# Kernel tuning notes

Measured on AMD Instinct MI355X. Metric: run time of the kernel, lower is better.

## Reference

```python
import jax, jax.numpy as jnp
import numpy as np

H, B, N, D = 8, 256, 200, 128
KD = D // H                      # key_dim = embed_dim // n_heads = 16
TRI = N * (N - 1) // 2           # strictly upper-triangular count per matrix
NORM = 1.0 / np.sqrt(KD)
NEG = -jnp.inf


def setup_inputs() -> dict:
    key = jax.random.key(0)
    k1, k2, k3, k4, k5 = jax.random.split(key, 5)
    q = jax.random.normal(k1, (B, N, D), dtype=jnp.float32)
    che_mask = jax.random.randint(k2, (H, B, TRI), 0, 2).astype(bool)
    exchange = jax.random.randint(k3, (B, 2), 0, N)
    stdv = 1.0 / np.sqrt(KD)
    Wq = jax.random.uniform(k4, (H, D, KD), jnp.float32, -stdv, stdv)
    Wk = jax.random.uniform(k5, (H, D, KD), jnp.float32, -stdv, stdv)
    return {"q": q, "che_mask": che_mask, "exchange": exchange, "Wq": Wq, "Wk": Wk}


def reference(q, che_mask, exchange, Wq, Wk):
    # Q, K: (H, B, N, KD)
    Q = jnp.einsum('bnd,hdk->hbnk', q, Wq)
    K = jnp.einsum('bnd,hdk->hbnk', q, Wk)
    # tanh-rescaled scores: (H, B, N, N)
    comp = jnp.tanh(NORM * jnp.einsum('hbik,hbjk->hbij', Q, K)) * 10.0

    # 1) lower triangle (incl. diagonal) -> -inf
    tril = jnp.tril(jnp.ones((N, N), dtype=bool))
    comp = jnp.where(tril, NEG, comp)

    # 2) strictly-upper positions where che_mask == 0 -> -inf
    # torch boolean indexing enumerates ~tril elements row-major == triu_indices order
    iu0, iu1 = np.triu_indices(N, k=1)
    keep = jnp.zeros((H, B, N, N), dtype=bool).at[:, :, iu0, iu1].set(che_mask)
    comp = jnp.where(jnp.logical_and(~tril, ~keep), NEG, comp)

    # 3) last 28 query rows fully masked
    comp = comp.at[:, :, -28:, :].set(NEG)

    # 4) per-batch exchange-pair scatter on head 0 only
    b_idx = jnp.arange(B)
    comp = comp.at[0, b_idx, exchange[:, 1], exchange[:, 0]].set(NEG)
    comp = comp.at[0, b_idx, exchange[:, 0], exchange[:, 1]].set(NEG)

    # 5) fixed column 100 masked
    comp = comp.at[:, :, :, 100].set(NEG)

    # global (flattened over N*N) softmax / log_softmax per (head, batch)
    im = comp.reshape(H, B, N * N)
    return jax.nn.log_softmax(im, axis=-1), jax.nn.softmax(im, axis=-1)
```

## Files before the change

### kernel.cpp

```cpp
#include <hip/hip_runtime.h>
#include <math.h>

#define Hh 8
#define Bb 256
#define Nn 200
#define Dd 128
#define KDk 16
#define TRI_ 19900
#define NN_ 40000
#define OUT_HALF 81920000ull
#define QK_FLOATS 6553600

#define NEG_FIN (-1.0e30f)

__device__ __forceinline__ float fast_exp2(float x) {
#if __has_builtin(__builtin_amdgcn_exp2f)
  return __builtin_amdgcn_exp2f(x);
#else
  return exp2f(x);
#endif
}
__device__ __forceinline__ float fast_log2(float x) {
#if __has_builtin(__builtin_amdgcn_logf)
  return __builtin_amdgcn_logf(x);
#else
  return log2f(x);
#endif
}
__device__ __forceinline__ float fast_rcp(float x) {
#if __has_builtin(__builtin_amdgcn_rcpf)
  return __builtin_amdgcn_rcpf(x);
#else
  return 1.0f / x;
#endif
}

__device__ __forceinline__ float dot16(float4 a0, float4 a1, float4 a2, float4 a3,
                                       float4 b0, float4 b1, float4 b2, float4 b3) {
  return a0.x*b0.x + a0.y*b0.y + a0.z*b0.z + a0.w*b0.w
       + a1.x*b1.x + a1.y*b1.y + a1.z*b1.z + a1.w*b1.w
       + a2.x*b2.x + a2.y*b2.y + a2.z*b2.z + a2.w*b2.w
       + a3.x*b3.x + a3.y*b3.y + a3.z*b3.z + a3.w*b3.w;
}

__global__ void k_detect(const unsigned char* __restrict__ che, int* __restrict__ flag) {
  const int t = threadIdx.x;
  unsigned char a4 = 0, a8 = 0;
  #pragma unroll
  for (int k = 0; k < 16; ++k) {
    const int i = t * 16 + k;
    const unsigned char v = che[i];
    if (i & 3) a4 |= v;
    else if (i & 7) a8 |= v;
  }
  const unsigned long long m4 = __ballot(a4 != 0);
  const unsigned long long m8 = __ballot(a8 != 0);
  if (t == 0) *flag = m4 ? 1 : (m8 ? 4 : 8);
}

__global__ __launch_bounds__(256) void k_fill(float* __restrict__ out) {
  const int hb = blockIdx.x;
  const int lane = threadIdx.x & 63;
  const int wave = threadIdx.x >> 6;
  float* __restrict__ oLS = out + (size_t)hb * NN_;
  float* __restrict__ oSM = out + OUT_HALF + (size_t)hb * NN_;
  const float4 vneg = make_float4(NEG_FIN, NEG_FIN, NEG_FIN, NEG_FIN);
  const float4 vzer = make_float4(0.0f, 0.0f, 0.0f, 0.0f);
  #pragma unroll 1
  for (int t = 0; t < 50; ++t) {
    const int r = wave + 4 * t;
    const int qlo = (r < 172) ? ((r + 1) >> 2) : 50;
    if (lane < qlo) {
      const size_t ro = (size_t)r * 200 + 4 * lane;
      *(float4*)(oLS + ro) = vneg;
      *(float4*)(oSM + ro) = vzer;
    }
  }
}

__global__ __launch_bounds__(256) void k_proj(const float* __restrict__ q,
    const float* __restrict__ Wq, const float* __restrict__ Wk,
    float* __restrict__ Qg, float* __restrict__ Kg) {
  __shared__ float As[64 * 132];
  __shared__ float Bst[128 * 68];
  const int tid = threadIdx.x;
  const int r0 = blockIdx.x * 64;

  const float4* src = (const float4*)q;
  #pragma unroll
  for (int p = 0; p < 8; ++p) {
    const int t2 = tid + p * 256;
    const int row = t2 >> 5, q4 = t2 & 31;
    float4 v = src[(size_t)(r0 + row) * 32 + q4];
    *(float4*)&As[row * 132 + q4 * 4] = v;
  }

  #pragma unroll 1
  for (int ct = 0; ct < 4; ++ct) {
    const int c0 = ct * 64;
    __syncthreads();
    #pragma unroll
    for (int p = 0; p < 8; ++p) {
      const int t2 = tid + p * 256;
      const int d = t2 >> 4, qd = t2 & 15;
      const int c = c0 + qd * 4;
      const int h = c >> 5, m = (c >> 4) & 1, kk0 = c & 15;
      const float* Wsrc = m ? Wk : Wq;
      const float4 v = *(const float4*)&Wsrc[(h * 128 + d) * 16 + kk0];
      *(float4*)&Bst[d * 68 + qd * 4] = v;
    }
    __syncthreads();

    const int tn = tid >> 4;
    const int tc = tid & 15;
    float acc[4][4] = {};
    #pragma unroll
    for (int dq = 0; dq < 32; ++dq) {
      float a[4][4];
      #pragma unroll
      for (int r = 0; r < 4; ++r) {
        float4 t = *(const float4*)&As[(tn * 4 + r) * 132 + dq * 4];
        a[r][0] = t.x; a[r][1] = t.y; a[r][2] = t.z; a[r][3] = t.w;
      }
      #pragma unroll
      for (int dd = 0; dd < 4; ++dd) {
        float4 bv = *(const float4*)&Bst[(dq * 4 + dd) * 68 + tc * 4];
        #pragma unroll
        for (int r = 0; r < 4; ++r) {
          acc[r][0] += a[r][dd] * bv.x;
          acc[r][1] += a[r][dd] * bv.y;
          acc[r][2] += a[r][dd] * bv.z;
          acc[r][3] += a[r][dd] * bv.w;
        }
      }
    }
    const int cq = c0 + tc * 4;
    const int h = cq >> 5, m = (cq >> 4) & 1, kkb = cq & 15;
    float* dst = m ? Kg : Qg;
    #pragma unroll
    for (int r = 0; r < 4; ++r) {
      const int nrow = r0 + tn * 4 + r;
      const int b = nrow / 200, n = nrow - b * 200;
      float4 v = make_float4(acc[r][0], acc[r][1], acc[r][2], acc[r][3]);
      *(float4*)(dst + (size_t)((h * 256 + b) * 200 + n) * 16 + kkb) = v;
    }
  }
}

__global__ __launch_bounds__(512, 4) void k_attn(
    const float* __restrict__ Qg, const float* __restrict__ Kg,
    const unsigned char* __restrict__ che, const int* __restrict__ exch,
    const int* __restrict__ flag, float* __restrict__ out) {
  const int hb = blockIdx.x;
  const int h = hb >> 8, b = hb & 255;
  const int tid = threadIdx.x;
  const int lane = tid & 63;
  const int wave = __builtin_amdgcn_readfirstlane(tid >> 6);
  const float* __restrict__ Qb = Qg + (size_t)hb * 3200;
  const float* __restrict__ Kb = Kg + (size_t)hb * 3200;
  const int cs = *flag;
  const unsigned char* __restrict__ cheB = che + (size_t)hb * (size_t)TRI_ * (size_t)cs;
  const int e0 = exch[2 * b], e1 = exch[2 * b + 1];
  const int emin = min(e0, e1), emax = max(e0, e1);
  const bool h0 = (h == 0);

  __shared__ float red[8];
  __shared__ unsigned char cheS[19904];

  const float C2E = 0.72134752044448f;
  const float L2E = 1.44269504088896f;

  if (cs == 1) {
    const unsigned int* srcp = (const unsigned int*)cheB;
    unsigned int* dst = (unsigned int*)cheS;
    for (int o = tid; o < TRI_ / 4; o += 512) dst[o] = srcp[o];
  } else if (cs == 4) {
    const uint4* srcp = (const uint4*)cheB;
    unsigned int* dst = (unsigned int*)cheS;
    for (int o = tid; o < TRI_ / 4; o += 512) {
      const uint4 v = srcp[o];
      dst[o] = (v.x ? 1u : 0u) | ((v.y ? 1u : 0u) << 8)
             | ((v.z ? 1u : 0u) << 16) | ((v.w ? 1u : 0u) << 24);
    }
  } else {
    for (int o = tid; o < TRI_; o += 512) cheS[o] = cheB[(size_t)o * 8];
  }

  const int kq = (lane < 50) ? lane : 49;
  float4 kr[4][4];
  #pragma unroll
  for (int c = 0; c < 4; ++c) {
    const float4* kp = (const float4*)(Kb + (size_t)(4 * kq + c) * 16);
    kr[c][0] = kp[0]; kr[c][1] = kp[1]; kr[c][2] = kp[2]; kr[c][3] = kp[3];
  }
  __syncthreads();

  float psum = 0.0f;
  const int ntB = (wave < 4) ? 22 : 21;
  #pragma unroll 1
  for (int t = 0; t < ntB; ++t) {
    const int r = wave + 8 * t;
    const int base = r * 199 - ((r * (r - 1)) >> 1) - r - 1;
    const float4* qp = (const float4*)(Qb + (size_t)r * 16);
    const float4 q0 = qp[0], q1 = qp[1], q2 = qp[2], q3 = qp[3];
    if (lane < 50 && 4 * lane + 3 > r) {
      #pragma unroll
      for (int c = 0; c < 4; ++c) {
        const int j = 4 * lane + c;
        int live = ((j > r) & (j != 100)) ? 1 : 0;
        const int idx = live ? (base + j) : 0;
        live &= (cheS[idx] != 0) ? 1 : 0;
        if (h0 && (r == emin) && (j == emax)) live = 0;
        const float d = dot16(q0, q1, q2, q3, kr[c][0], kr[c][1], kr[c][2], kr[c][3]);
        const float E = fast_exp2(C2E * d);
        const float s10 = -20.0f * fast_rcp(E + 1.0f);
        psum += live ? fast_exp2(L2E * s10) : 0.0f;
      }
    }
  }

  #pragma unroll
  for (int o = 32; o > 0; o >>= 1) psum += __shfl_xor(psum, o, 64);
  if (lane == 0) red[wave] = psum;
  __syncthreads();
  float Z = 0.0f;
  #pragma unroll
  for (int w2 = 0; w2 < 8; ++w2) Z += red[w2];
  const float lnZ = 0.69314718056f * fast_log2(Z);

  const size_t obase = (size_t)hb * NN_;
  float* __restrict__ oLS = out + obase;
  float* __restrict__ oSM = out + OUT_HALF + obase;

  #pragma unroll 1
  for (int t = 0; t < ntB; ++t) {
    const int r = wave + 8 * t;
    const int qlo = (r + 1) >> 2;
    const int base = r * 199 - ((r * (r - 1)) >> 1) - r - 1;
    const float4* qp = (const float4*)(Qb + (size_t)r * 16);
    const float4 q0 = qp[0], q1 = qp[1], q2 = qp[2], q3 = qp[3];
    float lsv[4], smv[4];
    #pragma unroll
    for (int c = 0; c < 4; ++c) {
      const int j = 4 * lane + c;
      int live = ((j > r) & (j != 100) & (j < 200)) ? 1 : 0;
      const int idx = live ? (base + j) : 0;
      live &= (cheS[idx] != 0) ? 1 : 0;
      if (h0 && (r == emin) && (j == emax)) live = 0;
      const float d = dot16(q0, q1, q2, q3, kr[c][0], kr[c][1], kr[c][2], kr[c][3]);
      const float E = fast_exp2(C2E * d);
      const float s10 = -20.0f * fast_rcp(E + 1.0f);
      const float ls = s10 - lnZ;
      lsv[c] = live ? ls : NEG_FIN;
      smv[c] = live ? fast_exp2(L2E * ls) : 0.0f;
    }
    if (lane >= qlo && lane < 50) {
      const size_t ro = (size_t)r * 200 + 4 * lane;
      *(float4*)(oLS + ro) = make_float4(lsv[0], lsv[1], lsv[2], lsv[3]);
      *(float4*)(oSM + ro) = make_float4(smv[0], smv[1], smv[2], smv[3]);
    }
  }
}

extern "C" void kernel_launch(void* const* d_in, const int* in_sizes, int n_in,
                              void* d_out, int out_size, void* d_ws, size_t ws_size,
                              hipStream_t stream) {
  const float* q           = (const float*)d_in[0];
  const unsigned char* che = (const unsigned char*)d_in[1];
  const int* exch          = (const int*)d_in[2];
  const float* Wq          = (const float*)d_in[3];
  const float* Wk          = (const float*)d_in[4];
  float* out = (float*)d_out;
  float* ws  = (float*)d_ws;

  const size_t need = (size_t)(4 + 2 * QK_FLOATS) * sizeof(float);
  int* flag = (int*)ws;
  float* Qg = ws + 4;
  float* Kg = Qg + QK_FLOATS;

  if (ws_size < need) {
    k_detect<<<dim3(1), dim3(64), 0, stream>>>(che, flag);
    return;
  }

  k_detect<<<dim3(1), dim3(64), 0, stream>>>(che, flag);
  k_fill<<<dim3(2048), dim3(256), 0, stream>>>(out);
  k_proj<<<dim3(800), dim3(256), 0, stream>>>(q, Wq, Wk, Qg, Kg);
  k_attn<<<dim3(2048), dim3(512), 0, stream>>>(Qg, Kg, che, exch, flag, out);
}
```

Measured before the change: 1.075 ms.

## Remap attention lanes to column pairs and split projection across grid y

The attention kernel now gives each lane two key columns per segment, split into two segments by column range, instead of four columns across 50 lanes. Rows whose columns all lie past the first segment are skipped, so the wasted idle lanes (50 of 64 active) shrink. Stores become float2 instead of float4. The projection kernel moves its four column tiles into a second grid dimension for more parallel blocks, and k_attn launch bounds rise to 6 waves per SIMD, which may limit registers.

Result: faster. 1.052 ms (-2.2%).

```diff
diff --git a/kernel.cpp b/kernel.cpp
--- a/kernel.cpp
+++ b/kernel.cpp
@@ -85,6 +85,7 @@
   __shared__ float Bst[128 * 68];
   const int tid = threadIdx.x;
   const int r0 = blockIdx.x * 64;
+  const int c0 = blockIdx.y * 64;
 
   const float4* src = (const float4*)q;
   #pragma unroll
@@ -94,60 +95,54 @@
     float4 v = src[(size_t)(r0 + row) * 32 + q4];
     *(float4*)&As[row * 132 + q4 * 4] = v;
   }
-
-  #pragma unroll 1
-  for (int ct = 0; ct < 4; ++ct) {
-    const int c0 = ct * 64;
-    __syncthreads();
+  #pragma unroll
+  for (int p = 0; p < 8; ++p) {
+    const int t2 = tid + p * 256;
+    const int d = t2 >> 4, qd = t2 & 15;
+    const int c = c0 + qd * 4;
+    const int h = c >> 5, m = (c >> 4) & 1, kk0 = c & 15;
+    const float* Wsrc = m ? Wk : Wq;
+    const float4 v = *(const float4*)&Wsrc[(h * 128 + d) * 16 + kk0];
+    *(float4*)&Bst[d * 68 + qd * 4] = v;
+  }
+  __syncthreads();
+
+  const int tn = tid >> 4;
+  const int tc = tid & 15;
+  float acc[4][4] = {};
+  #pragma unroll
+  for (int dq = 0; dq < 32; ++dq) {
+    float a[4][4];
     #pragma unroll
-    for (int p = 0; p < 8; ++p) {
-      const int t2 = tid + p * 256;
-      const int d = t2 >> 4, qd = t2 & 15;
-      const int c = c0 + qd * 4;
-      const int h = c >> 5, m = (c >> 4) & 1, kk0 = c & 15;
-      const float* Wsrc = m ? Wk : Wq;
-      const float4 v = *(const float4*)&Wsrc[(h * 128 + d) * 16 + kk0];
-      *(float4*)&Bst[d * 68 + qd * 4] = v;
-    }
-    __syncthreads();
-
-    const int tn = tid >> 4;
-    const int tc = tid & 15;
-    float acc[4][4] = {};
+    for (int r = 0; r < 4; ++r) {
+      float4 t = *(const float4*)&As[(tn * 4 + r) * 132 + dq * 4];
+      a[r][0] = t.x; a[r][1] = t.y; a[r][2] = t.z; a[r][3] = t.w;
+    }
     #pragma unroll
-    for (int dq = 0; dq < 32; ++dq) {
-      float a[4][4];
+    for (int dd = 0; dd < 4; ++dd) {
+      float4 bv = *(const float4*)&Bst[(dq * 4 + dd) * 68 + tc * 4];
       #pragma unroll
       for (int r = 0; r < 4; ++r) {
-        float4 t = *(const float4*)&As[(tn * 4 + r) * 132 + dq * 4];
-        a[r][0] = t.x; a[r][1] = t.y; a[r][2] = t.z; a[r][3] = t.w;
+        acc[r][0] += a[r][dd] * bv.x;
+        acc[r][1] += a[r][dd] * bv.y;
+        acc[r][2] += a[r][dd] * bv.z;
+        acc[r][3] += a[r][dd] * bv.w;
       }
-      #pragma unroll
-      for (int dd = 0; dd < 4; ++dd) {
-        float4 bv = *(const float4*)&Bst[(dq * 4 + dd) * 68 + tc * 4];
-        #pragma unroll
-        for (int r = 0; r < 4; ++r) {
-          acc[r][0] += a[r][dd] * bv.x;
-          acc[r][1] += a[r][dd] * bv.y;
-          acc[r][2] += a[r][dd] * bv.z;
-          acc[r][3] += a[r][dd] * bv.w;
-        }
-      }
-    }
-    const int cq = c0 + tc * 4;
-    const int h = cq >> 5, m = (cq >> 4) & 1, kkb = cq & 15;
-    float* dst = m ? Kg : Qg;
-    #pragma unroll
-    for (int r = 0; r < 4; ++r) {
-      const int nrow = r0 + tn * 4 + r;
-      const int b = nrow / 200, n = nrow - b * 200;
-      float4 v = make_float4(acc[r][0], acc[r][1], acc[r][2], acc[r][3]);
-      *(float4*)(dst + (size_t)((h * 256 + b) * 200 + n) * 16 + kkb) = v;
-    }
-  }
-}
-
-__global__ __launch_bounds__(512, 4) void k_attn(
+    }
+  }
+  const int cq = c0 + tc * 4;
+  const int h = cq >> 5, m = (cq >> 4) & 1, kkb = cq & 15;
+  float* dst = m ? Kg : Qg;
+  #pragma unroll
+  for (int r = 0; r < 4; ++r) {
+    const int nrow = r0 + tn * 4 + r;
+    const int b = nrow / 200, n = nrow - b * 200;
+    float4 v = make_float4(acc[r][0], acc[r][1], acc[r][2], acc[r][3]);
+    *(float4*)(dst + (size_t)((h * 256 + b) * 200 + n) * 16 + kkb) = v;
+  }
+}
+
+__global__ __launch_bounds__(512, 6) void k_attn(
     const float* __restrict__ Qg, const float* __restrict__ Kg,
     const unsigned char* __restrict__ che, const int* __restrict__ exch,
     const int* __restrict__ flag, float* __restrict__ out) {
@@ -185,37 +180,41 @@
   } else {
     for (int o = tid; o < TRI_; o += 512) cheS[o] = cheB[(size_t)o * 8];
   }
-
-  const int kq = (lane < 50) ? lane : 49;
-  float4 kr[4][4];
-  #pragma unroll
-  for (int c = 0; c < 4; ++c) {
-    const float4* kp = (const float4*)(Kb + (size_t)(4 * kq + c) * 16);
-    kr[c][0] = kp[0]; kr[c][1] = kp[1]; kr[c][2] = kp[2]; kr[c][3] = kp[3];
-  }
   __syncthreads();
 
+  const int tB0 = (134 - wave) >> 3;
+  const int tB1 = (wave < 4) ? 22 : 21;
+
   float psum = 0.0f;
-  const int ntB = (wave < 4) ? 22 : 21;
   #pragma unroll 1
-  for (int t = 0; t < ntB; ++t) {
-    const int r = wave + 8 * t;
-    const int base = r * 199 - ((r * (r - 1)) >> 1) - r - 1;
-    const float4* qp = (const float4*)(Qb + (size_t)r * 16);
-    const float4 q0 = qp[0], q1 = qp[1], q2 = qp[2], q3 = qp[3];
-    if (lane < 50 && 4 * lane + 3 > r) {
-      #pragma unroll
-      for (int c = 0; c < 4; ++c) {
-        const int j = 4 * lane + c;
-        int live = ((j > r) & (j != 100)) ? 1 : 0;
-        const int idx = live ? (base + j) : 0;
-        live &= (cheS[idx] != 0) ? 1 : 0;
-        if (h0 && (r == emin) && (j == emax)) live = 0;
-        const float d = dot16(q0, q1, q2, q3, kr[c][0], kr[c][1], kr[c][2], kr[c][3]);
-        const float E = fast_exp2(C2E * d);
-        const float s10 = -20.0f * fast_rcp(E + 1.0f);
-        psum += live ? fast_exp2(L2E * s10) : 0.0f;
-      }
+  for (int seg = 0; seg < 2; ++seg) {
+    const int p = seg * 64 + lane;
+    const int j0 = 2 * p, j1 = j0 + 1;
+    const int j0c = min(j0, 199), j1c = min(j1, 199);
+    const float4* ka = (const float4*)(Kb + (size_t)j0c * 16);
+    const float4 a0 = ka[0], a1 = ka[1], a2 = ka[2], a3 = ka[3];
+    const float4* kb = (const float4*)(Kb + (size_t)j1c * 16);
+    const float4 b0 = kb[0], b1 = kb[1], b2 = kb[2], b3 = kb[3];
+    const int v0 = ((j0 < 200) & (j0 != 100)) ? 1 : 0;
+    const int v1 = ((j1 < 200) & (j1 != 100)) ? 1 : 0;
+    const int tB = seg ? tB1 : tB0;
+    #pragma unroll 2
+    for (int t = 0; t < tB; ++t) {
+      const int r = wave + 8 * t;
+      const int base = r * 199 - ((r * (r - 1)) >> 1) - r - 1;
+      const float4* qp = (const float4*)(Qb + (size_t)r * 16);
+      const float4 q0 = qp[0], q1 = qp[1], q2 = qp[2], q3 = qp[3];
+      int l0 = v0 & ((j0 > r) ? 1 : 0);
+      int l1 = v1 & ((j1 > r) ? 1 : 0);
+      l0 &= (cheS[l0 ? (base + j0) : 0] != 0) ? 1 : 0;
+      l1 &= (cheS[l1 ? (base + j1) : 0] != 0) ? 1 : 0;
+      if (h0 && (r == emin)) { if (j0 == emax) l0 = 0; if (j1 == emax) l1 = 0; }
+      const float d0 = dot16(q0, q1, q2, q3, a0, a1, a2, a3);
+      const float d1 = dot16(q0, q1, q2, q3, b0, b1, b2, b3);
+      const float s0 = -20.0f * fast_rcp(fast_exp2(C2E * d0) + 1.0f);
+      const float s1 = -20.0f * fast_rcp(fast_exp2(C2E * d1) + 1.0f);
+      psum += l0 ? fast_exp2(L2E * s0) : 0.0f;
+      psum += l1 ? fast_exp2(L2E * s1) : 0.0f;
     }
   }
 
@@ -233,31 +232,43 @@
   float* __restrict__ oSM = out + OUT_HALF + obase;
 
   #pragma unroll 1
-  for (int t = 0; t < ntB; ++t) {
-    const int r = wave + 8 * t;
-    const int qlo = (r + 1) >> 2;
-    const int base = r * 199 - ((r * (r - 1)) >> 1) - r - 1;
-    const float4* qp = (const float4*)(Qb + (size_t)r * 16);
-    const float4 q0 = qp[0], q1 = qp[1], q2 = qp[2], q3 = qp[3];
-    float lsv[4], smv[4];
-    #pragma unroll
-    for (int c = 0; c < 4; ++c) {
-      const int j = 4 * lane + c;
-      int live = ((j > r) & (j != 100) & (j < 200)) ? 1 : 0;
-      const int idx = live ? (base + j) : 0;
-      live &= (cheS[idx] != 0) ? 1 : 0;
-      if (h0 && (r == emin) && (j == emax)) live = 0;
-      const float d = dot16(q0, q1, q2, q3, kr[c][0], kr[c][1], kr[c][2], kr[c][3]);
-      const float E = fast_exp2(C2E * d);
-      const float s10 = -20.0f * fast_rcp(E + 1.0f);
-      const float ls = s10 - lnZ;
-      lsv[c] = live ? ls : NEG_FIN;
-      smv[c] = live ? fast_exp2(L2E * ls) : 0.0f;
-    }
-    if (lane >= qlo && lane < 50) {
-      const size_t ro = (size_t)r * 200 + 4 * lane;
-      *(float4*)(oLS + ro) = make_float4(lsv[0], lsv[1], lsv[2], lsv[3]);
-      *(float4*)(oSM + ro) = make_float4(smv[0], smv[1], smv[2], smv[3]);
+  for (int seg = 0; seg < 2; ++seg) {
+    const int p = seg * 64 + lane;
+    const int j0 = 2 * p, j1 = j0 + 1;
+    const int j0c = min(j0, 199), j1c = min(j1, 199);
+    const float4* ka = (const float4*)(Kb + (size_t)j0c * 16);
+    const float4 a0 = ka[0], a1 = ka[1], a2 = ka[2], a3 = ka[3];
+    const float4* kb = (const float4*)(Kb + (size_t)j1c * 16);
+    const float4 b0 = kb[0], b1 = kb[1], b2 = kb[2], b3 = kb[3];
+    const int v0 = ((j0 < 200) & (j0 != 100)) ? 1 : 0;
+    const int v1 = ((j1 < 200) & (j1 != 100)) ? 1 : 0;
+    const int canst = seg ? ((lane <= 35) ? 1 : 0) : 1;
+    const int tB = seg ? tB1 : tB0;
+    #pragma unroll 2
+    for (int t = 0; t < tB; ++t) {
+      const int r = wave + 8 * t;
+      const int base = r * 199 - ((r * (r - 1)) >> 1) - r - 1;
+      const float4* qp = (const float4*)(Qb + (size_t)r * 16);
+      const float4 q0 = qp[0], q1 = qp[1], q2 = qp[2], q3 = qp[3];
+      int l0 = v0 & ((j0 > r) ? 1 : 0);
+      int l1 = v1 & ((j1 > r) ? 1 : 0);
+      l0 &= (cheS[l0 ? (base + j0) : 0] != 0) ? 1 : 0;
+      l1 &= (cheS[l1 ? (base + j1) : 0] != 0) ? 1 : 0;
+      if (h0 && (r == emin)) { if (j0 == emax) l0 = 0; if (j1 == emax) l1 = 0; }
+      const float d0 = dot16(q0, q1, q2, q3, a0, a1, a2, a3);
+      const float d1 = dot16(q0, q1, q2, q3, b0, b1, b2, b3);
+      const float s0 = -20.0f * fast_rcp(fast_exp2(C2E * d0) + 1.0f);
+      const float s1 = -20.0f * fast_rcp(fast_exp2(C2E * d1) + 1.0f);
+      const float ls0 = l0 ? (s0 - lnZ) : NEG_FIN;
+      const float ls1 = l1 ? (s1 - lnZ) : NEG_FIN;
+      const float sm0 = l0 ? fast_exp2(L2E * (s0 - lnZ)) : 0.0f;
+      const float sm1 = l1 ? fast_exp2(L2E * (s1 - lnZ)) : 0.0f;
+      const int qlo2 = ((r + 1) >> 2) << 1;
+      if (canst && p >= qlo2) {
+        const size_t ro = (size_t)r * 200 + 2 * p;
+        *(float2*)(oLS + ro) = make_float2(ls0, ls1);
+        *(float2*)(oSM + ro) = make_float2(sm0, sm1);
+      }
     }
   }
 }
@@ -285,6 +296,6 @@
 
   k_detect<<<dim3(1), dim3(64), 0, stream>>>(che, flag);
   k_fill<<<dim3(2048), dim3(256), 0, stream>>>(out);
-  k_proj<<<dim3(800), dim3(256), 0, stream>>>(q, Wq, Wk, Qg, Kg);
+  k_proj<<<dim3(800, 4), dim3(256), 0, stream>>>(q, Wq, Wk, Qg, Kg);
   k_attn<<<dim3(2048), dim3(512), 0, stream>>>(Qg, Kg, che, exch, flag, out);
 }
```
